# Kernel tuning notes

Hardware: AMD Instinct MI355X
Metric: run time of the kernel (lower is better)

Reference implementation:

```python
import jax, jax.numpy as jnp
import numpy as np

B, L, W, H = 16, 256, 4, 128
N = L + W - 1  # 259
EPS = 1e-6


def setup_inputs() -> dict:
    key = jax.random.key(0)
    k1, k2 = jax.random.split(key)
    x1 = jax.random.normal(k1, (B, 1, N, H), dtype=jnp.float32)
    x2 = jax.random.normal(k2, (B, 1, N, H), dtype=jnp.float32)
    return {"x1": x1, "x2": x2}


def _attention_matrix(x1, x2):
    # x1: (B,1,n,d); x2.permute(0,2,1,3): (B,n,1,d) -> broadcast diff (B,n,n,d)
    diff = x1 - jnp.transpose(x2, (0, 2, 1, 3))
    euclid = jnp.sqrt(jnp.sum(diff * diff, axis=3) + EPS)  # (B,n,n)
    return 1.0 / (euclid + 1.0)


def _wp(x, a):
    # x: (B,1,n,H), a: (B,n) -> weighted sliding-window sum over W positions
    wx = x * a[:, None, :, None]  # (B,1,n,H)
    out = wx[:, :, 0:L, :]
    for k in range(1, W):  # small fixed loop over filter width
        out = out + wx[:, :, k:k + L, :]
    return out  # (B,1,L,H)


def reference(x1, x2):
    att = _attention_matrix(x1, x2)      # (B,n,n)
    x1_a = jnp.sum(att, axis=1)          # (B,n) weight per x1 position
    x2_a = jnp.sum(att, axis=2)          # (B,n) weight per x2 position
    return (_wp(x1, x1_a), _wp(x2, x2_a))
```

## Files before the change

### kernel.cpp

```cpp
#include <hip/hip_runtime.h>
#include <hip/hip_bf16.h>
#include <math.h>

#define Bn  16
#define Ln  256
#define Wn  4
#define Hn  128
#define Nn  259
#define EPSF 1e-6f
#define NB  (Bn * Nn)

typedef float f32x4 __attribute__((ext_vector_type(4)));
typedef short s16x8 __attribute__((ext_vector_type(8)));


__global__ __launch_bounds__(256) void prep(const float* __restrict__ x1,
                                            const float* __restrict__ x2,
                                            float* __restrict__ ws) {
    const int wid  = (blockIdx.x * 256 + threadIdx.x) >> 6;
    const int lane = threadIdx.x & 63;
    if (wid >= 2 * NB) return;
    const bool one = (wid < NB);
    const float* x = one ? x1 : x2;
    const int    r = one ? wid : wid - NB;
    const float2 v = ((const float2*)(x + (size_t)r * Hn))[lane];
    union { __hip_bfloat16 h; unsigned short u; } c0, c1;
    c0.h = __float2bfloat16(v.x);
    c1.h = __float2bfloat16(v.y);
    unsigned short* xb = (unsigned short*)(ws + 4 * NB) + (one ? 0 : (size_t)NB * Hn);
    ((unsigned int*)(xb + (size_t)r * Hn))[lane] =
        (unsigned int)c0.u | ((unsigned int)c1.u << 16);
    const float a0 = __bfloat162float(c0.h), a1 = __bfloat162float(c1.h);
    float s = a0 * a0 + a1 * a1;
    #pragma unroll
    for (int off = 32; off; off >>= 1) s += __shfl_down(s, off);
    if (lane == 0) {
        ws[wid]          = 0.f;
        ws[2 * NB + wid] = s;
    }
}

__global__ __launch_bounds__(256) void att_mfma(float* __restrict__ ws) {
    __shared__ unsigned short As[64 * 136];
    __shared__ unsigned short Bs[64 * 136];
    __shared__ float n2s[64], n1s[64];

    float*       x1a = ws;
    float*       x2a = ws + NB;
    const float* n1g = ws + 2 * NB;
    const float* n2g = ws + 3 * NB;
    const unsigned short* xb1 = (const unsigned short*)(ws + 4 * NB);
    const unsigned short* xb2 = xb1 + (size_t)NB * Hn;

    const int i0 = blockIdx.x * 64, j0 = blockIdx.y * 64, b = blockIdx.z;
    const int tid = threadIdx.x;

    for (int idx = tid; idx < 1024; idx += 256) {
        const int r = idx >> 4, c = idx & 15;
        uint4 va = make_uint4(0, 0, 0, 0), vb = va;
        if (i0 + r < Nn) va = ((const uint4*)(xb2 + (size_t)(b * Nn + i0 + r) * Hn))[c];
        if (j0 + r < Nn) vb = ((const uint4*)(xb1 + (size_t)(b * Nn + j0 + r) * Hn))[c];
        *((uint4*)&As[r * 136 + c * 8]) = va;
        *((uint4*)&Bs[r * 136 + c * 8]) = vb;
    }
    if (tid < 64)       n2s[tid]      = (i0 + tid < Nn)        ? n2g[b * Nn + i0 + tid]        : 0.f;
    else if (tid < 128) n1s[tid - 64] = (j0 + (tid - 64) < Nn) ? n1g[b * Nn + j0 + (tid - 64)] : 0.f;
    __syncthreads();

    const int w = tid >> 6, lane = tid & 63;
    const int rsel = lane & 15, q = lane >> 4;

    f32x4 acc[4] = {{0,0,0,0}, {0,0,0,0}, {0,0,0,0}, {0,0,0,0}};
    const unsigned short* arow = &As[(w * 16 + rsel) * 136 + q * 8];
    const unsigned short* brow = &Bs[rsel * 136 + q * 8];
    #pragma unroll
    for (int s = 0; s < 4; ++s) {
        const s16x8 af = *((const s16x8*)(arow + s * 32));
        #pragma unroll
        for (int t = 0; t < 4; ++t) {
            const s16x8 bf = *((const s16x8*)(brow + t * 16 * 136 + s * 32));
            acc[t] = __builtin_amdgcn_mfma_f32_16x16x32_bf16(af, bf, acc[t], 0, 0, 0);
        }
    }

    float rowacc[4] = {0.f, 0.f, 0.f, 0.f};
    #pragma unroll
    for (int t = 0; t < 4; ++t) {
        const int   j   = j0 + t * 16 + rsel;
        const bool  jv  = (j < Nn);
        const float n1v = n1s[t * 16 + rsel];
        float cp = 0.f;
        #pragma unroll
        for (int reg = 0; reg < 4; ++reg) {
            const int   i   = i0 + w * 16 + q * 4 + reg;
            const float e   = fmaf(-2.f, acc[t][reg], n2s[w * 16 + q * 4 + reg] + n1v + EPSF);
            const float att = ((i < Nn) && jv) ? 1.f / (sqrtf(e) + 1.f) : 0.f;
            rowacc[reg] += att;
            cp          += att;
        }
        cp += __shfl_xor(cp, 16);
        cp += __shfl_xor(cp, 32);
        if (q == 0 && jv) atomicAdd(&x1a[b * Nn + j], cp);
    }
    #pragma unroll
    for (int reg = 0; reg < 4; ++reg) {
        float rs = rowacc[reg];
        #pragma unroll
        for (int off = 8; off; off >>= 1) rs += __shfl_down(rs, off, 16);
        const int i = i0 + w * 16 + q * 4 + reg;
        if (rsel == 0 && i < Nn) atomicAdd(&x2a[b * Nn + i], rs);
    }
}

__global__ __launch_bounds__(256) void wp_kernel(const float* __restrict__ x1,
                                                 const float* __restrict__ x2,
                                                 const float* __restrict__ ws,
                                                 float* __restrict__ out) {
    const int PER = Bn * Ln * Hn / 4;
    int g = blockIdx.x * 256 + threadIdx.x;
    const float* x; const float* a; float4* o; int e;
    if (g < PER) { x = x1; a = ws;      o = (float4*)out;       e = g; }
    else         { x = x2; a = ws + NB; o = (float4*)out + PER; e = g - PER; }

    const int b   = e >> 13;
    const int rem = e & 8191;
    const int l   = rem >> 5;
    const int h4  = rem & 31;

    const float4* xb = (const float4*)(x + (size_t)b * Nn * Hn);
    float4 acc = make_float4(0.f, 0.f, 0.f, 0.f);
    #pragma unroll
    for (int k = 0; k < Wn; ++k) {
        const float  av = a[b * Nn + l + k];
        const float4 xv = xb[(l + k) * (Hn / 4) + h4];
        acc.x += av * xv.x;
        acc.y += av * xv.y;
        acc.z += av * xv.z;
        acc.w += av * xv.w;
    }
    o[e] = acc;
}

extern "C" void kernel_launch(void* const* d_in, const int* in_sizes, int n_in,
                              void* d_out, int out_size, void* d_ws, size_t ws_size,
                              hipStream_t stream) {
    const float* x1 = (const float*)d_in[0];
    const float* x2 = (const float*)d_in[1];
    float* ws = (float*)d_ws;

    prep<<<(2 * NB + 3) / 4, 256, 0, stream>>>(x1, x2, ws);

    dim3 gridA(5, 5, Bn);
    att_mfma<<<gridA, 256, 0, stream>>>(ws);

    const int total_f4 = 2 * Bn * Ln * Hn / 4;
    wp_kernel<<<total_f4 / 256, 256, 0, stream>>>(x1, x2, ws, (float*)d_out);
}
```

Measured before the change: 70.54 us.

## Fuse three kernels into one cooperative kernel with grid-wide syncs

Replaces the prep, attention-MFMA and window-sum kernels with a single cooperative kernel of 512 blocks that runs the three phases separated by grid.sync(). The goal is to cut the launch overhead and inter-kernel gaps of three small back-to-back launches. In exchange it pays two grid-wide barriers, and only 400 of the 512 blocks do work in the attention phase. Occupancy must also allow every block to be resident at once.

```diff
diff --git a/kernel.cpp b/kernel.cpp
--- a/kernel.cpp
+++ b/kernel.cpp
@@ -1,6 +1,9 @@
 #include <hip/hip_runtime.h>
 #include <hip/hip_bf16.h>
+#include <hip/hip_cooperative_groups.h>
 #include <math.h>
+
+namespace cg = cooperative_groups;
 
 #define Bn  16
 #define Ln  256
@@ -9,38 +12,16 @@
 #define Nn  259
 #define EPSF 1e-6f
 #define NB  (Bn * Nn)
+#define GRIDB 512
 
 typedef float f32x4 __attribute__((ext_vector_type(4)));
 typedef short s16x8 __attribute__((ext_vector_type(8)));
 
 
-__global__ __launch_bounds__(256) void prep(const float* __restrict__ x1,
-                                            const float* __restrict__ x2,
-                                            float* __restrict__ ws) {
-    const int wid  = (blockIdx.x * 256 + threadIdx.x) >> 6;
-    const int lane = threadIdx.x & 63;
-    if (wid >= 2 * NB) return;
-    const bool one = (wid < NB);
-    const float* x = one ? x1 : x2;
-    const int    r = one ? wid : wid - NB;
-    const float2 v = ((const float2*)(x + (size_t)r * Hn))[lane];
-    union { __hip_bfloat16 h; unsigned short u; } c0, c1;
-    c0.h = __float2bfloat16(v.x);
-    c1.h = __float2bfloat16(v.y);
-    unsigned short* xb = (unsigned short*)(ws + 4 * NB) + (one ? 0 : (size_t)NB * Hn);
-    ((unsigned int*)(xb + (size_t)r * Hn))[lane] =
-        (unsigned int)c0.u | ((unsigned int)c1.u << 16);
-    const float a0 = __bfloat162float(c0.h), a1 = __bfloat162float(c1.h);
-    float s = a0 * a0 + a1 * a1;
-    #pragma unroll
-    for (int off = 32; off; off >>= 1) s += __shfl_down(s, off);
-    if (lane == 0) {
-        ws[wid]          = 0.f;
-        ws[2 * NB + wid] = s;
-    }
-}
-
-__global__ __launch_bounds__(256) void att_mfma(float* __restrict__ ws) {
+__global__ __launch_bounds__(256, 2) void fused(const float* __restrict__ x1,
+                                                const float* __restrict__ x2,
+                                                float* __restrict__ ws,
+                                                float* __restrict__ out) {
     __shared__ unsigned short As[64 * 136];
     __shared__ unsigned short Bs[64 * 136];
     __shared__ float n2s[64], n1s[64];
@@ -49,96 +30,124 @@
     float*       x2a = ws + NB;
     const float* n1g = ws + 2 * NB;
     const float* n2g = ws + 3 * NB;
-    const unsigned short* xb1 = (const unsigned short*)(ws + 4 * NB);
-    const unsigned short* xb2 = xb1 + (size_t)NB * Hn;
+    unsigned short* xb1 = (unsigned short*)(ws + 4 * NB);
+    unsigned short* xb2 = xb1 + (size_t)NB * Hn;
 
-    const int i0 = blockIdx.x * 64, j0 = blockIdx.y * 64, b = blockIdx.z;
-    const int tid = threadIdx.x;
+    const int tid  = threadIdx.x;
+    const int lane = tid & 63;
 
-    for (int idx = tid; idx < 1024; idx += 256) {
-        const int r = idx >> 4, c = idx & 15;
-        uint4 va = make_uint4(0, 0, 0, 0), vb = va;
-        if (i0 + r < Nn) va = ((const uint4*)(xb2 + (size_t)(b * Nn + i0 + r) * Hn))[c];
-        if (j0 + r < Nn) vb = ((const uint4*)(xb1 + (size_t)(b * Nn + j0 + r) * Hn))[c];
-        *((uint4*)&As[r * 136 + c * 8]) = va;
-        *((uint4*)&Bs[r * 136 + c * 8]) = vb;
-    }
-    if (tid < 64)       n2s[tid]      = (i0 + tid < Nn)        ? n2g[b * Nn + i0 + tid]        : 0.f;
-    else if (tid < 128) n1s[tid - 64] = (j0 + (tid - 64) < Nn) ? n1g[b * Nn + j0 + (tid - 64)] : 0.f;
-    __syncthreads();
-
-    const int w = tid >> 6, lane = tid & 63;
-    const int rsel = lane & 15, q = lane >> 4;
-
-    f32x4 acc[4] = {{0,0,0,0}, {0,0,0,0}, {0,0,0,0}, {0,0,0,0}};
-    const unsigned short* arow = &As[(w * 16 + rsel) * 136 + q * 8];
-    const unsigned short* brow = &Bs[rsel * 136 + q * 8];
-    #pragma unroll
-    for (int s = 0; s < 4; ++s) {
-        const s16x8 af = *((const s16x8*)(arow + s * 32));
+    const int wave0 = (blockIdx.x << 2) | (tid >> 6);
+    for (int wid = wave0; wid < 2 * NB; wid += GRIDB * 4) {
+        const bool one = (wid < NB);
+        const float* x = one ? x1 : x2;
+        const int    r = one ? wid : wid - NB;
+        const float2 v = ((const float2*)(x + (size_t)r * Hn))[lane];
+        union { __hip_bfloat16 h; unsigned short u; } c0, c1;
+        c0.h = __float2bfloat16(v.x);
+        c1.h = __float2bfloat16(v.y);
+        unsigned short* xb = one ? xb1 : xb2;
+        ((unsigned int*)(xb + (size_t)r * Hn))[lane] =
+            (unsigned int)c0.u | ((unsigned int)c1.u << 16);
+        const float a0 = __bfloat162float(c0.h), a1 = __bfloat162float(c1.h);
+        float s = a0 * a0 + a1 * a1;
         #pragma unroll
-        for (int t = 0; t < 4; ++t) {
-            const s16x8 bf = *((const s16x8*)(brow + t * 16 * 136 + s * 32));
-            acc[t] = __builtin_amdgcn_mfma_f32_16x16x32_bf16(af, bf, acc[t], 0, 0, 0);
+        for (int off = 32; off; off >>= 1) s += __shfl_down(s, off);
+        if (lane == 0) {
+            ws[wid]          = 0.f;
+            ws[2 * NB + wid] = s;
         }
     }
 
-    float rowacc[4] = {0.f, 0.f, 0.f, 0.f};
-    #pragma unroll
-    for (int t = 0; t < 4; ++t) {
-        const int   j   = j0 + t * 16 + rsel;
-        const bool  jv  = (j < Nn);
-        const float n1v = n1s[t * 16 + rsel];
-        float cp = 0.f;
+    cg::this_grid().sync();
+
+    if (blockIdx.x < 400) {
+        const int b   = blockIdx.x / 25;
+        const int rem = blockIdx.x % 25;
+        const int i0  = (rem / 5) * 64;
+        const int j0  = (rem % 5) * 64;
+
+        for (int idx = tid; idx < 1024; idx += 256) {
+            const int r = idx >> 4, c = idx & 15;
+            uint4 va = make_uint4(0, 0, 0, 0), vb = va;
+            if (i0 + r < Nn) va = ((const uint4*)(xb2 + (size_t)(b * Nn + i0 + r) * Hn))[c];
+            if (j0 + r < Nn) vb = ((const uint4*)(xb1 + (size_t)(b * Nn + j0 + r) * Hn))[c];
+            *((uint4*)&As[r * 136 + c * 8]) = va;
+            *((uint4*)&Bs[r * 136 + c * 8]) = vb;
+        }
+        if (tid < 64)       n2s[tid]      = (i0 + tid < Nn)        ? n2g[b * Nn + i0 + tid]        : 0.f;
+        else if (tid < 128) n1s[tid - 64] = (j0 + (tid - 64) < Nn) ? n1g[b * Nn + j0 + (tid - 64)] : 0.f;
+        __syncthreads();
+
+        const int w = tid >> 6, rsel = lane & 15, q = lane >> 4;
+
+        f32x4 acc[4] = {{0,0,0,0}, {0,0,0,0}, {0,0,0,0}, {0,0,0,0}};
+        const unsigned short* arow = &As[(w * 16 + rsel) * 136 + q * 8];
+        const unsigned short* brow = &Bs[rsel * 136 + q * 8];
+        #pragma unroll
+        for (int s = 0; s < 4; ++s) {
+            const s16x8 af = *((const s16x8*)(arow + s * 32));
+            #pragma unroll
+            for (int t = 0; t < 4; ++t) {
+                const s16x8 bf = *((const s16x8*)(brow + t * 16 * 136 + s * 32));
+                acc[t] = __builtin_amdgcn_mfma_f32_16x16x32_bf16(af, bf, acc[t], 0, 0, 0);
+            }
+        }
+
+        float rowacc[4] = {0.f, 0.f, 0.f, 0.f};
+        #pragma unroll
+        for (int t = 0; t < 4; ++t) {
+            const int   j   = j0 + t * 16 + rsel;
+            const bool  jv  = (j < Nn);
+            const float n1v = n1s[t * 16 + rsel];
+            float cp = 0.f;
+            #pragma unroll
+            for (int reg = 0; reg < 4; ++reg) {
+                const int   i   = i0 + w * 16 + q * 4 + reg;
+                const float e   = fmaf(-2.f, acc[t][reg], n2s[w * 16 + q * 4 + reg] + n1v + EPSF);
+                const float att = ((i < Nn) && jv) ? 1.f / (sqrtf(e) + 1.f) : 0.f;
+                rowacc[reg] += att;
+                cp          += att;
+            }
+            cp += __shfl_xor(cp, 16);
+            cp += __shfl_xor(cp, 32);
+            if (q == 0 && jv) atomicAdd(&x1a[b * Nn + j], cp);
+        }
         #pragma unroll
         for (int reg = 0; reg < 4; ++reg) {
-            const int   i   = i0 + w * 16 + q * 4 + reg;
-            const float e   = fmaf(-2.f, acc[t][reg], n2s[w * 16 + q * 4 + reg] + n1v + EPSF);
-            const float att = ((i < Nn) && jv) ? 1.f / (sqrtf(e) + 1.f) : 0.f;
-            rowacc[reg] += att;
-            cp          += att;
+            float rs = rowacc[reg];
+            #pragma unroll
+            for (int off = 8; off; off >>= 1) rs += __shfl_down(rs, off, 16);
+            const int i = i0 + w * 16 + q * 4 + reg;
+            if (rsel == 0 && i < Nn) atomicAdd(&x2a[b * Nn + i], rs);
         }
-        cp += __shfl_xor(cp, 16);
-        cp += __shfl_xor(cp, 32);
-        if (q == 0 && jv) atomicAdd(&x1a[b * Nn + j], cp);
     }
-    #pragma unroll
-    for (int reg = 0; reg < 4; ++reg) {
-        float rs = rowacc[reg];
+
+    cg::this_grid().sync();
+
+    const int PER = Bn * Ln * Hn / 4;
+    for (int g = blockIdx.x * 256 + tid; g < 2 * PER; g += GRIDB * 256) {
+        const float* x; const float* a; float4* o; int e;
+        if (g < PER) { x = x1; a = x1a; o = (float4*)out;       e = g; }
+        else         { x = x2; a = x2a; o = (float4*)out + PER; e = g - PER; }
+
+        const int b   = e >> 13;
+        const int rem = e & 8191;
+        const int l   = rem >> 5;
+        const int h4  = rem & 31;
+
+        const float4* xb = (const float4*)(x + (size_t)b * Nn * Hn);
+        float4 accv = make_float4(0.f, 0.f, 0.f, 0.f);
         #pragma unroll
-        for (int off = 8; off; off >>= 1) rs += __shfl_down(rs, off, 16);
-        const int i = i0 + w * 16 + q * 4 + reg;
-        if (rsel == 0 && i < Nn) atomicAdd(&x2a[b * Nn + i], rs);
+        for (int k = 0; k < Wn; ++k) {
+            const float  av = a[b * Nn + l + k];
+            const float4 xv = xb[(l + k) * (Hn / 4) + h4];
+            accv.x += av * xv.x;
+            accv.y += av * xv.y;
+            accv.z += av * xv.z;
+            accv.w += av * xv.w;
+        }
+        o[e] = accv;
     }
-}
-
-__global__ __launch_bounds__(256) void wp_kernel(const float* __restrict__ x1,
-                                                 const float* __restrict__ x2,
-                                                 const float* __restrict__ ws,
-                                                 float* __restrict__ out) {
-    const int PER = Bn * Ln * Hn / 4;
-    int g = blockIdx.x * 256 + threadIdx.x;
-    const float* x; const float* a; float4* o; int e;
-    if (g < PER) { x = x1; a = ws;      o = (float4*)out;       e = g; }
-    else         { x = x2; a = ws + NB; o = (float4*)out + PER; e = g - PER; }
-
-    const int b   = e >> 13;
-    const int rem = e & 8191;
-    const int l   = rem >> 5;
-    const int h4  = rem & 31;
-
-    const float4* xb = (const float4*)(x + (size_t)b * Nn * Hn);
-    float4 acc = make_float4(0.f, 0.f, 0.f, 0.f);
-    #pragma unroll
-    for (int k = 0; k < Wn; ++k) {
-        const float  av = a[b * Nn + l + k];
-        const float4 xv = xb[(l + k) * (Hn / 4) + h4];
-        acc.x += av * xv.x;
-        acc.y += av * xv.y;
-        acc.z += av * xv.z;
-        acc.w += av * xv.w;
-    }
-    o[e] = acc;
 }
 
 extern "C" void kernel_launch(void* const* d_in, const int* in_sizes, int n_in,
@@ -146,13 +155,10 @@
                               hipStream_t stream) {
     const float* x1 = (const float*)d_in[0];
     const float* x2 = (const float*)d_in[1];
-    float* ws = (float*)d_ws;
+    float* ws   = (float*)d_ws;
+    float* outp = (float*)d_out;
 
-    prep<<<(2 * NB + 3) / 4, 256, 0, stream>>>(x1, x2, ws);
-
-    dim3 gridA(5, 5, Bn);
-    att_mfma<<<gridA, 256, 0, stream>>>(ws);
-
-    const int total_f4 = 2 * Bn * Ln * Hn / 4;
-    wp_kernel<<<total_f4 / 256, 256, 0, stream>>>(x1, x2, ws, (float*)d_out);
+    void* args[] = { (void*)&x1, (void*)&x2, (void*)&ws, (void*)&outp };
+    hipLaunchCooperativeKernel((const void*)fused, dim3(GRIDB), dim3(256),
+                               args, 0, stream);
 }
```

New measurement: 168.0 us. 2.38x slower.

## Fuse bf16 conversion and norms into attention kernel, replace atomics with partials

Applied to the files above, without the earlier changes.

Removes the separate prep kernel. The attention kernel now converts the fp32 inputs to bf16 directly into shared memory and computes the squared row norms with extra MFMA self-products (diagonal of A·Aᵀ). Global atomics for the row and column sums are replaced by per-tile partial sums written to a padded workspace. The window-product kernel reduces the five partials per position into shared memory before applying the sliding window. This saves a launch and a global bf16 round trip and avoids atomic contention and zero-initialisation, at the cost of redundant fp32 loads and conversions across tiles plus a small reduction in the final kernel.

```diff
diff --git a/kernel.cpp b/kernel.cpp
--- a/kernel.cpp
+++ b/kernel.cpp
@@ -8,80 +8,77 @@
 #define Hn  128
 #define Nn  259
 #define EPSF 1e-6f
-#define NB  (Bn * Nn)
+#define PSTR 320
+#define X2AP_OFF (5 * Bn * PSTR)
 
 typedef float f32x4 __attribute__((ext_vector_type(4)));
 typedef short s16x8 __attribute__((ext_vector_type(8)));
 
+__device__ __forceinline__ unsigned short bfb(float x) {
+    union { __hip_bfloat16 h; unsigned short u; } t;
+    t.h = __float2bfloat16(x);
+    return t.u;
+}
 
-__global__ __launch_bounds__(256) void prep(const float* __restrict__ x1,
+__global__ __launch_bounds__(256) void att2(const float* __restrict__ x1,
                                             const float* __restrict__ x2,
                                             float* __restrict__ ws) {
-    const int wid  = (blockIdx.x * 256 + threadIdx.x) >> 6;
-    const int lane = threadIdx.x & 63;
-    if (wid >= 2 * NB) return;
-    const bool one = (wid < NB);
-    const float* x = one ? x1 : x2;
-    const int    r = one ? wid : wid - NB;
-    const float2 v = ((const float2*)(x + (size_t)r * Hn))[lane];
-    union { __hip_bfloat16 h; unsigned short u; } c0, c1;
-    c0.h = __float2bfloat16(v.x);
-    c1.h = __float2bfloat16(v.y);
-    unsigned short* xb = (unsigned short*)(ws + 4 * NB) + (one ? 0 : (size_t)NB * Hn);
-    ((unsigned int*)(xb + (size_t)r * Hn))[lane] =
-        (unsigned int)c0.u | ((unsigned int)c1.u << 16);
-    const float a0 = __bfloat162float(c0.h), a1 = __bfloat162float(c1.h);
-    float s = a0 * a0 + a1 * a1;
-    #pragma unroll
-    for (int off = 32; off; off >>= 1) s += __shfl_down(s, off);
-    if (lane == 0) {
-        ws[wid]          = 0.f;
-        ws[2 * NB + wid] = s;
-    }
-}
-
-__global__ __launch_bounds__(256) void att_mfma(float* __restrict__ ws) {
     __shared__ unsigned short As[64 * 136];
     __shared__ unsigned short Bs[64 * 136];
     __shared__ float n2s[64], n1s[64];
+    __shared__ float colpart[4 * 64];
 
-    float*       x1a = ws;
-    float*       x2a = ws + NB;
-    const float* n1g = ws + 2 * NB;
-    const float* n2g = ws + 3 * NB;
-    const unsigned short* xb1 = (const unsigned short*)(ws + 4 * NB);
-    const unsigned short* xb2 = xb1 + (size_t)NB * Hn;
-
-    const int i0 = blockIdx.x * 64, j0 = blockIdx.y * 64, b = blockIdx.z;
+    const int it = blockIdx.x, jt = blockIdx.y, b = blockIdx.z;
+    const int i0 = it * 64, j0 = jt * 64;
     const int tid = threadIdx.x;
 
-    for (int idx = tid; idx < 1024; idx += 256) {
-        const int r = idx >> 4, c = idx & 15;
-        uint4 va = make_uint4(0, 0, 0, 0), vb = va;
-        if (i0 + r < Nn) va = ((const uint4*)(xb2 + (size_t)(b * Nn + i0 + r) * Hn))[c];
-        if (j0 + r < Nn) vb = ((const uint4*)(xb1 + (size_t)(b * Nn + j0 + r) * Hn))[c];
-        *((uint4*)&As[r * 136 + c * 8]) = va;
-        *((uint4*)&Bs[r * 136 + c * 8]) = vb;
+    const float* __restrict__ x1b = x1 + (size_t)b * Nn * Hn;
+    const float* __restrict__ x2b = x2 + (size_t)b * Nn * Hn;
+
+    #pragma unroll
+    for (int iter = 0; iter < 8; ++iter) {
+        const int idx = iter * 256 + tid;
+        const int r = idx >> 5, c4 = idx & 31;
+        float4 va = make_float4(0.f, 0.f, 0.f, 0.f), vb = va;
+        if (i0 + r < Nn) va = ((const float4*)(x2b + (i0 + r) * Hn))[c4];
+        if (j0 + r < Nn) vb = ((const float4*)(x1b + (j0 + r) * Hn))[c4];
+        const unsigned long long pa =
+            (unsigned long long)bfb(va.x)        | ((unsigned long long)bfb(va.y) << 16) |
+            ((unsigned long long)bfb(va.z) << 32) | ((unsigned long long)bfb(va.w) << 48);
+        const unsigned long long pb =
+            (unsigned long long)bfb(vb.x)        | ((unsigned long long)bfb(vb.y) << 16) |
+            ((unsigned long long)bfb(vb.z) << 32) | ((unsigned long long)bfb(vb.w) << 48);
+        *((unsigned long long*)&As[r * 136 + c4 * 4]) = pa;
+        *((unsigned long long*)&Bs[r * 136 + c4 * 4]) = pb;
     }
-    if (tid < 64)       n2s[tid]      = (i0 + tid < Nn)        ? n2g[b * Nn + i0 + tid]        : 0.f;
-    else if (tid < 128) n1s[tid - 64] = (j0 + (tid - 64) < Nn) ? n1g[b * Nn + j0 + (tid - 64)] : 0.f;
     __syncthreads();
 
     const int w = tid >> 6, lane = tid & 63;
     const int rsel = lane & 15, q = lane >> 4;
 
     f32x4 acc[4] = {{0,0,0,0}, {0,0,0,0}, {0,0,0,0}, {0,0,0,0}};
-    const unsigned short* arow = &As[(w * 16 + rsel) * 136 + q * 8];
-    const unsigned short* brow = &Bs[rsel * 136 + q * 8];
+    f32x4 accA = {0,0,0,0}, accB = {0,0,0,0};
+    const unsigned short* arow  = &As[(w * 16 + rsel) * 136 + q * 8];
+    const unsigned short* bnrow = &Bs[(w * 16 + rsel) * 136 + q * 8];
+    const unsigned short* brow  = &Bs[rsel * 136 + q * 8];
     #pragma unroll
     for (int s = 0; s < 4; ++s) {
         const s16x8 af = *((const s16x8*)(arow + s * 32));
+        const s16x8 bn = *((const s16x8*)(bnrow + s * 32));
+        accA = __builtin_amdgcn_mfma_f32_16x16x32_bf16(af, af, accA, 0, 0, 0);
+        accB = __builtin_amdgcn_mfma_f32_16x16x32_bf16(bn, bn, accB, 0, 0, 0);
         #pragma unroll
         for (int t = 0; t < 4; ++t) {
             const s16x8 bf = *((const s16x8*)(brow + t * 16 * 136 + s * 32));
             acc[t] = __builtin_amdgcn_mfma_f32_16x16x32_bf16(af, bf, acc[t], 0, 0, 0);
         }
     }
+
+    if (q == (rsel >> 2)) {
+        n2s[w * 16 + rsel] = accA[rsel & 3];
+        n1s[w * 16 + rsel] = accB[rsel & 3];
+    }
+    __syncthreads();
 
     float rowacc[4] = {0.f, 0.f, 0.f, 0.f};
     #pragma unroll
@@ -100,7 +97,7 @@
         }
         cp += __shfl_xor(cp, 16);
         cp += __shfl_xor(cp, 32);
-        if (q == 0 && jv) atomicAdd(&x1a[b * Nn + j], cp);
+        if (q == 0) colpart[w * 64 + t * 16 + rsel] = cp;
     }
     #pragma unroll
     for (int reg = 0; reg < 4; ++reg) {
@@ -108,7 +105,15 @@
         #pragma unroll
         for (int off = 8; off; off >>= 1) rs += __shfl_down(rs, off, 16);
         const int i = i0 + w * 16 + q * 4 + reg;
-        if (rsel == 0 && i < Nn) atomicAdd(&x2a[b * Nn + i], rs);
+        if (rsel == 0 && i < Nn)
+            ws[X2AP_OFF + (jt * Bn + b) * PSTR + i] = rs;
+    }
+    __syncthreads();
+    if (tid < 64) {
+        const int j = j0 + tid;
+        if (j < Nn)
+            ws[(it * Bn + b) * PSTR + j] =
+                colpart[tid] + colpart[64 + tid] + colpart[128 + tid] + colpart[192 + tid];
     }
 }
 
@@ -116,29 +121,40 @@
                                                  const float* __restrict__ x2,
                                                  const float* __restrict__ ws,
                                                  float* __restrict__ out) {
+    __shared__ float a_s[11];
     const int PER = Bn * Ln * Hn / 4;
-    int g = blockIdx.x * 256 + threadIdx.x;
-    const float* x; const float* a; float4* o; int e;
-    if (g < PER) { x = x1; a = ws;      o = (float4*)out;       e = g; }
-    else         { x = x2; a = ws + NB; o = (float4*)out + PER; e = g - PER; }
+    const int blk = blockIdx.x;
+    const bool second = blk >= 512;
+    const int eb = (second ? blk - 512 : blk) * 256;
+    const int b  = eb >> 13;
+    const int l0 = (eb & 8191) >> 5;
 
-    const int b   = e >> 13;
-    const int rem = e & 8191;
-    const int l   = rem >> 5;
-    const int h4  = rem & 31;
+    const float* x = second ? x2 : x1;
+    const float* p = ws + (second ? X2AP_OFF : 0) + b * PSTR;
+    if (threadIdx.x < 11) {
+        const int j = l0 + threadIdx.x;
+        float s = 0.f;
+        #pragma unroll
+        for (int t = 0; t < 5; ++t) s += p[t * (Bn * PSTR) + j];
+        a_s[threadIdx.x] = s;
+    }
+    __syncthreads();
 
+    const int e  = eb + threadIdx.x;
+    const int l  = (e & 8191) >> 5;
+    const int h4 = e & 31;
     const float4* xb = (const float4*)(x + (size_t)b * Nn * Hn);
     float4 acc = make_float4(0.f, 0.f, 0.f, 0.f);
     #pragma unroll
     for (int k = 0; k < Wn; ++k) {
-        const float  av = a[b * Nn + l + k];
+        const float  av = a_s[l - l0 + k];
         const float4 xv = xb[(l + k) * (Hn / 4) + h4];
         acc.x += av * xv.x;
         acc.y += av * xv.y;
         acc.z += av * xv.z;
         acc.w += av * xv.w;
     }
-    o[e] = acc;
+    ((float4*)out)[(second ? PER : 0) + e] = acc;
 }
 
 extern "C" void kernel_launch(void* const* d_in, const int* in_sizes, int n_in,
@@ -148,11 +164,8 @@
     const float* x2 = (const float*)d_in[1];
     float* ws = (float*)d_ws;
 
-    prep<<<(2 * NB + 3) / 4, 256, 0, stream>>>(x1, x2, ws);
+    dim3 gridA(5, 5, Bn);
+    att2<<<gridA, 256, 0, stream>>>(x1, x2, ws);
 
-    dim3 gridA(5, 5, Bn);
-    att_mfma<<<gridA, 256, 0, stream>>>(ws);
-
-    const int total_f4 = 2 * Bn * Ln * Hn / 4;
-    wp_kernel<<<total_f4 / 256, 256, 0, stream>>>(x1, x2, ws, (float*)d_out);
+    wp_kernel<<<1024, 256, 0, stream>>>(x1, x2, ws, (float*)d_out);
 }
```

Result: no change. 70.17 us (-0.5%).
